# Optimization experiments

Hardware: AMD Instinct MI355X
Metric: run time of the kernel (lower is better)

The kernel has to match this reference:

```python
import jax, jax.numpy as jnp
import numpy as np
import math

B, TD, TP, D, H = 16, 256, 1024, 512, 8
DH = D // H
G_MIN = 0.05
LN_EPS = 1e-5
SCALE = 1.0 / math.sqrt(DH)


def _ln(x, g, b):
    m = jnp.mean(x, axis=-1, keepdims=True)
    v = jnp.var(x, axis=-1, keepdims=True)
    return (x - m) * jax.lax.rsqrt(v + LN_EPS) * g + b


def _evi(x, w1, b1, w2, b2, k):
    # EvidentialHead: Linear -> SiLU -> Linear(d->4), NIG params -> gate
    h = jax.nn.silu(x @ w1 + b1)
    p = h @ w2 + b2  # (B,T,4)
    gamma, nu, alpha, beta = jnp.split(p, 4, axis=-1)
    nu = jax.nn.softplus(nu) + 1e-6
    alpha = jax.nn.softplus(alpha) + 1.0
    beta = jax.nn.softplus(beta) + 1e-6
    sigma2 = beta / (nu * (alpha - 1.0))  # (B,T,1)
    g = jnp.clip(jnp.exp(-k * sigma2[..., 0]), G_MIN, 1.0)  # (B,T)
    return g


def _xattn(Q, KV, log_bias, wq, bq, wk, bk, wv, bv, wo, bo, lng, lnb):
    # Q: (B,M,D), KV: (B,N,D), log_bias: (B,N) added to logits pre-softmax
    Bq, M, _ = Q.shape
    N = KV.shape[1]
    q = (Q @ wq + bq).reshape(Bq, M, H, DH)
    k_ = (KV @ wk + bk).reshape(Bq, N, H, DH)
    v = (KV @ wv + bv).reshape(Bq, N, H, DH)
    scores = jnp.einsum('bmhd,bnhd->bhmn', q, k_) * SCALE
    scores = scores + log_bias[:, None, None, :]
    attn = jax.nn.softmax(scores, axis=-1)
    out = jnp.einsum('bhmn,bnhd->bmhd', attn, v).reshape(Bq, M, D)
    out = out @ wo + bo
    return _ln(Q + out, lng, lnb)


def _ffn(x, w1, b1, w2, b2, lng, lnb):
    # Linear(d,4d) -> SiLU -> Linear(4d,d) -> LayerNorm (no residual)
    h = jax.nn.silu(x @ w1 + b1)
    return _ln(h @ w2 + b2, lng, lnb)


def setup_inputs() -> dict:
    key = jax.random.key(0)
    ks = iter(jax.random.split(key, 64))

    def w(shape, s=0.02):
        return s * jax.random.normal(next(ks), shape, jnp.float32)

    def attn_params(pfx):
        p = {}
        for nm in ('wq', 'wk', 'wv', 'wo'):
            p[pfx + '_' + nm] = w((D, D))
        for nm in ('bq', 'bk', 'bv', 'bo'):
            p[pfx + '_' + nm] = jnp.zeros((D,), jnp.float32)
        p[pfx + '_lng'] = jnp.ones((D,), jnp.float32)
        p[pfx + '_lnb'] = jnp.zeros((D,), jnp.float32)
        return p

    def ffn_params(pfx):
        return {pfx + '_w1': w((D, 4 * D)), pfx + '_b1': jnp.zeros((4 * D,), jnp.float32),
                pfx + '_w2': w((4 * D, D)), pfx + '_b2': jnp.zeros((D,), jnp.float32),
                pfx + '_lng': jnp.ones((D,), jnp.float32), pfx + '_lnb': jnp.zeros((D,), jnp.float32)}

    inp = {
        'Hd': jax.random.normal(next(ks), (B, TD, D), jnp.float32),
        'Hp': jax.random.normal(next(ks), (B, TP, D), jnp.float32),
        'k': 1,
        'evid_w1': w((D, D)), 'evid_b1': jnp.zeros((D,), jnp.float32),
        'evid_w2': w((D, 4)), 'evid_b2': jnp.zeros((4,), jnp.float32),
        'evip_w1': w((D, D)), 'evip_b1': jnp.zeros((D,), jnp.float32),
        'evip_w2': w((D, 4)), 'evip_b2': jnp.zeros((4,), jnp.float32),
    }
    inp.update(attn_params('p2d'))
    inp.update(attn_params('d2p'))
    inp.update(ffn_params('ffnd'))
    inp.update(ffn_params('ffnp'))
    return inp


def reference(Hd, Hp, k,
              evid_w1, evid_b1, evid_w2, evid_b2,
              evip_w1, evip_b1, evip_w2, evip_b2,
              p2d_wq, p2d_wk, p2d_wv, p2d_wo, p2d_bq, p2d_bk, p2d_bv, p2d_bo, p2d_lng, p2d_lnb,
              d2p_wq, d2p_wk, d2p_wv, d2p_wo, d2p_bq, d2p_bk, d2p_bv, d2p_bo, d2p_lng, d2p_lnb,
              ffnd_w1, ffnd_b1, ffnd_w2, ffnd_b2, ffnd_lng, ffnd_lnb,
              ffnp_w1, ffnp_b1, ffnp_w2, ffnp_b2, ffnp_lng, ffnp_lnb):
    gd = _evi(Hd, evid_w1, evid_b1, evid_w2, evid_b2, k)  # (B,TD)
    gp = _evi(Hp, evip_w1, evip_b1, evip_w2, evip_b2, k)  # (B,TP)
    Hp2 = _xattn(Hp, Hd, jnp.log(gd + 1e-12),
                 p2d_wq, p2d_bq, p2d_wk, p2d_bk, p2d_wv, p2d_bv, p2d_wo, p2d_bo, p2d_lng, p2d_lnb)
    Hd2 = _xattn(Hd, Hp, jnp.log(gp + 1e-12),
                 d2p_wq, d2p_bq, d2p_wk, d2p_bk, d2p_wv, d2p_bv, d2p_wo, d2p_bo, d2p_lng, d2p_lnb)
    Hd_out = _ffn(Hd2, ffnd_w1, ffnd_b1, ffnd_w2, ffnd_b2, ffnd_lng, ffnd_lnb)
    Hp_out = _ffn(Hp2, ffnp_w1, ffnp_b1, ffnp_w2, ffnp_b2, ffnp_lng, ffnp_lnb)
    return (Hd_out, Hp_out, gd, gp)
```

## Files before the change

kernel.cpp:

```cpp
#include <hip/hip_runtime.h>
#include <stdint.h>
#include <math.h>

typedef unsigned short u16;
typedef __attribute__((ext_vector_type(8))) short bf16x8;
typedef __attribute__((ext_vector_type(8))) short short8;
typedef __attribute__((ext_vector_type(4))) float f32x4;
typedef __attribute__((ext_vector_type(4))) unsigned short u16x4;

#define NB 16
#define TDr 256
#define TPr 1024
#define DM 512
#define NH 8
#define DHEAD 64

__device__ __forceinline__ float us2f(u16 u) {
  union { float f; unsigned int i; } x; x.i = ((unsigned int)u) << 16; return x.f;
}
__device__ __forceinline__ u16 f2us(float f) {
  union { float fl; unsigned int i; } x; x.fl = f;
  unsigned int u = x.i;
  return (u16)((u + 0x7fffu + ((u >> 16) & 1u)) >> 16);
}

__global__ __launch_bounds__(64) void detect_kernel(const u16* __restrict__ raw,
                                                    int* __restrict__ flag)
{
  const int lane = threadIdx.x;
  float mx = 0.f;
  for (int i = lane; i < 256; i += 64) {
    float v = us2f(raw[i]);
    v = fabsf(v);
    if (isfinite(v)) mx = fmaxf(mx, v); else mx = 1e30f;
  }
#pragma unroll
  for (int o = 32; o; o >>= 1) mx = fmaxf(mx, __shfl_xor(mx, o));
  if (lane == 0) flag[0] = (mx > 1e10f) ? 1 : 0;
}

struct CvtDesc { const void* src; unsigned long dst_off; int n; };
struct CvtTable { CvtDesc d[42]; };

__global__ __launch_bounds__(256) void cvt_kernel(CvtTable t, u16* __restrict__ base,
                                                  const int* __restrict__ flag)
{
  const CvtDesc d = t.d[blockIdx.y];
  u16* dst = base + d.dst_off;
  const int isf32 = flag[0];
  const int stride = gridDim.x * 256;
  const int tid0 = blockIdx.x * 256 + threadIdx.x;
  if (d.n >= 8) {
    const int n8 = d.n >> 3;
    if (isf32) {
      const float* s = (const float*)d.src;
      for (int i = tid0; i < n8; i += stride) {
        f32x4 a = *(const f32x4*)&s[i * 8];
        f32x4 b = *(const f32x4*)&s[i * 8 + 4];
        short8 o;
        o[0]=(short)f2us(a[0]); o[1]=(short)f2us(a[1]); o[2]=(short)f2us(a[2]); o[3]=(short)f2us(a[3]);
        o[4]=(short)f2us(b[0]); o[5]=(short)f2us(b[1]); o[6]=(short)f2us(b[2]); o[7]=(short)f2us(b[3]);
        *(short8*)&dst[i * 8] = o;
      }
    } else {
      const short8* s = (const short8*)d.src;
      for (int i = tid0; i < n8; i += stride) *(short8*)&dst[i * 8] = s[i];
    }
  } else {
    if (isf32) {
      const float* s = (const float*)d.src;
      for (int i = tid0; i < d.n; i += stride) dst[i] = f2us(s[i]);
    } else {
      const u16* s = (const u16*)d.src;
      for (int i = tid0; i < d.n; i += stride) dst[i] = s[i];
    }
  }
}

template<int BM, int BN>
__device__ __forceinline__ void gemm_core(
    const u16* __restrict__ Ab, const u16* __restrict__ Bb,
    int K, int tid, f32x4 (&acc)[BM/32][BN/32])
{
  constexpr int BK = 32;
  constexpr int FM = BM / 32;
  constexpr int FN = BN / 32;
  constexpr int LPT = (BM * BK / 8 + BN * BK / 8) / 256;
  __shared__ __align__(16) u16 As[2][BM * BK];
  __shared__ __align__(16) u16 Bs[2][BN * BK];

  const int lane = tid & 63;
  const int wm = (tid >> 6) >> 1;
  const int wn = (tid >> 6) & 1;

#pragma unroll
  for (int i = 0; i < FM; ++i)
#pragma unroll
    for (int j = 0; j < FN; ++j)
      acc[i][j] = (f32x4){0.f, 0.f, 0.f, 0.f};

  auto stage = [&](int buf, int k0) {
#pragma unroll
    for (int c = tid; c < BM * BK / 8; c += 256) {
      const int r  = c >> 2;
      const int kk = (c & 3) << 3;
      __builtin_amdgcn_global_load_lds(
          (const __attribute__((address_space(1))) uint32_t*)(Ab + (long)r * K + k0 + kk),
          (__attribute__((address_space(3))) uint32_t*)(&As[buf][c * 8]), 16, 0, 0);
    }
#pragma unroll
    for (int c = tid; c < BN * BK / 8; c += 256) {
      const int r  = c >> 2;
      const int kk = (c & 3) << 3;
      __builtin_amdgcn_global_load_lds(
          (const __attribute__((address_space(1))) uint32_t*)(Bb + (long)r * K + k0 + kk),
          (__attribute__((address_space(3))) uint32_t*)(&Bs[buf][c * 8]), 16, 0, 0);
    }
  };

  const int nt = K / BK;
  stage(0, 0);
  if (nt > 1) stage(1, BK);

  for (int t = 0; t < nt; ++t) {
    if (t + 1 < nt) {
      if constexpr (LPT == 4) asm volatile("s_waitcnt vmcnt(4)" ::: "memory");
      else                    asm volatile("s_waitcnt vmcnt(3)" ::: "memory");
    } else {
      asm volatile("s_waitcnt vmcnt(0)" ::: "memory");
    }
    asm volatile("s_barrier" ::: "memory");
    __builtin_amdgcn_sched_barrier(0);

    const int cur = t & 1;
    bf16x8 af[FM], bfv[FN];
#pragma unroll
    for (int i = 0; i < FM; ++i)
      af[i] = *(const bf16x8*)&As[cur][(wm * (BM/2) + i*16 + (lane & 15)) * BK + ((lane >> 4) << 3)];
#pragma unroll
    for (int j = 0; j < FN; ++j)
      bfv[j] = *(const bf16x8*)&Bs[cur][(wn * (BN/2) + j*16 + (lane & 15)) * BK + ((lane >> 4) << 3)];
#pragma unroll
    for (int i = 0; i < FM; ++i)
#pragma unroll
      for (int j = 0; j < FN; ++j)
        acc[i][j] = __builtin_amdgcn_mfma_f32_16x16x32_bf16(af[i], bfv[j], acc[i][j], 0, 0, 0);

    __builtin_amdgcn_sched_barrier(0);
    asm volatile("s_barrier" ::: "memory");
    __builtin_amdgcn_sched_barrier(0);
    if (t + 2 < nt) stage(cur, (t + 2) * BK);
  }
}

struct ProjSet {
  const u16 *A, *W, *bE, *bQ, *bK, *bV;
  u16 *H, *Q, *Kc, *VT;
  int ntokLog, mtiles;
};

__global__ __launch_bounds__(256) void proj_pair(ProjSet s0, ProjSet s1)
{
  const ProjSet S = blockIdx.z ? s1 : s0;
  if ((int)blockIdx.x >= S.mtiles) return;
  const int tid = threadIdx.x;
  const int lane = tid & 63;
  const int wm = (tid >> 6) >> 1, wn = (tid >> 6) & 1;
  const int r16 = lane & 15, rr4 = (lane >> 4) << 2;
  const long row0 = (long)blockIdx.x * 128;
  const long col0 = (long)blockIdx.y * 128;

  f32x4 acc[4][4];
  gemm_core<128,128>(S.A + row0 * 512, S.W + col0 * 512, 512, tid, acc);

  const int range = (int)(col0 >> 9);
  const u16* bp = range == 0 ? S.bE : range == 1 ? S.bQ : range == 2 ? S.bK : S.bV;
  u16* dst = range == 0 ? S.H : range == 1 ? S.Q : S.Kc;
  const int ntok = 1 << S.ntokLog;

#pragma unroll
  for (int i = 0; i < 4; ++i) {
    const long gr0 = row0 + wm*64 + i*16 + rr4;
#pragma unroll
    for (int j = 0; j < 4; ++j) {
      const int cr = (int)(col0 & 511) + wn*64 + j*16 + r16;
      const float badd = us2f(bp[cr]);
      if (range == 3) {
        const long b = gr0 >> S.ntokLog;
        const long t0 = gr0 & (ntok - 1);
        u16x4 pk;
#pragma unroll
        for (int r = 0; r < 4; ++r) pk[r] = f2us(acc[i][j][r] + badd);
        *(u16x4*)&S.VT[((long)b * 512 + cr) * ntok + t0] = pk;
      } else if (range == 0) {
#pragma unroll
        for (int r = 0; r < 4; ++r) {
          float v = acc[i][j][r] + badd;
          v = v / (1.f + __expf(-v));
          dst[(gr0 + r) * 512 + cr] = f2us(v);
        }
      } else {
#pragma unroll
        for (int r = 0; r < 4; ++r)
          dst[(gr0 + r) * 512 + cr] = f2us(acc[i][j][r] + badd);
      }
    }
  }
}

struct Gm { const u16* A; const u16* Bt; const u16* bias; u16* C; int mtiles; };

template<int SILU>
__global__ __launch_bounds__(256) void gemm_pair(Gm g0, Gm g1, int ldc, int K)
{
  const Gm G = blockIdx.z ? g1 : g0;
  if ((int)blockIdx.x >= G.mtiles) return;
  const int tid = threadIdx.x;
  const int lane = tid & 63;
  const int wm = (tid >> 6) >> 1, wn = (tid >> 6) & 1;
  const int r16 = lane & 15, rr4 = (lane >> 4) << 2;
  const long row0 = (long)blockIdx.x * 128;
  const long col0 = (long)blockIdx.y * 128;

  f32x4 acc[4][4];
  gemm_core<128,128>(G.A + row0 * (long)K, G.Bt + col0 * (long)K, K, tid, acc);

#pragma unroll
  for (int i = 0; i < 4; ++i) {
    const long gr0 = row0 + wm*64 + i*16 + rr4;
#pragma unroll
    for (int j = 0; j < 4; ++j) {
      const long gc = col0 + wn*64 + j*16 + r16;
      const float badd = us2f(G.bias[gc]);
#pragma unroll
      for (int r = 0; r < 4; ++r) {
        float v = acc[i][j][r] + badd;
        if (SILU) v = v / (1.f + __expf(-v));
        G.C[(gr0 + r) * (long)ldc + gc] = f2us(v);
      }
    }
  }
}

template<int NKV, int RPW>
__global__ __launch_bounds__(256) void attn_fused(
    const u16* __restrict__ Qp, const u16* __restrict__ Kp,
    const u16* __restrict__ Vt, const float* __restrict__ lb,
    u16* __restrict__ Aout, int M)
{
  constexpr int NC = NKV >> 7;
  constexpr int FI = RPW / 16;
  constexpr int NS = 4 * FI;
  constexpr int QT = 4 * RPW;
  constexpr int PLD = 136;
  __shared__ __align__(16) u16 Ps[4][RPW][PLD];

  const int tid  = threadIdx.x;
  const int lane = tid & 63;
  const int w    = tid >> 6;
  const int bh = blockIdx.y;
  const int b = bh >> 3, h = bh & 7;
  const long q0 = (long)blockIdx.x * QT;

  const u16* Qb = Qp + ((long)b * M + q0) * DM + h * DHEAD;
  const u16* Kb = Kp + (long)b * NKV * DM + h * DHEAD;
  const u16* Vb = Vt + ((long)b * DM + h * DHEAD) * NKV;
  const float* lbb = lb + (long)b * NKV;

  const int r16 = lane & 15;
  const int k8  = (lane >> 4) << 3;
  const int rr4 = (lane >> 4) << 2;
  const float SCALE = 0.125f;

  bf16x8 qa[FI][2];
#pragma unroll
  for (int i = 0; i < FI; ++i)
#pragma unroll
    for (int kc = 0; kc < 2; ++kc)
      qa[i][kc] = *(const bf16x8*)&Qb[(long)(w*RPW + i*16 + r16) * DM + kc*32 + k8];

  f32x4 acc_o[FI][4];
#pragma unroll
  for (int i = 0; i < FI; ++i)
#pragma unroll
    for (int jo = 0; jo < 4; ++jo)
      acc_o[i][jo] = (f32x4){0.f, 0.f, 0.f, 0.f};
  float mrow[NS], lrow[NS];
#pragma unroll
  for (int s = 0; s < NS; ++s) { mrow[s] = -1e30f; lrow[s] = 0.f; }

#pragma unroll
  for (int c = 0; c < NC; ++c) {
    const int t0 = c * 128;
    f32x4 acc_s[FI][8];
#pragma unroll
    for (int i = 0; i < FI; ++i)
#pragma unroll
      for (int j = 0; j < 8; ++j)
        acc_s[i][j] = (f32x4){0.f, 0.f, 0.f, 0.f};
#pragma unroll
    for (int j = 0; j < 8; ++j) {
      const long trow = t0 + j*16 + r16;
      bf16x8 kb0 = *(const bf16x8*)&Kb[trow * DM + k8];
      bf16x8 kb1 = *(const bf16x8*)&Kb[trow * DM + 32 + k8];
#pragma unroll
      for (int i = 0; i < FI; ++i) {
        acc_s[i][j] = __builtin_amdgcn_mfma_f32_16x16x32_bf16(qa[i][0], kb0, acc_s[i][j], 0, 0, 0);
        acc_s[i][j] = __builtin_amdgcn_mfma_f32_16x16x32_bf16(qa[i][1], kb1, acc_s[i][j], 0, 0, 0);
      }
    }

    float lbv[8];
#pragma unroll
    for (int j = 0; j < 8; ++j) lbv[j] = lbb[t0 + j*16 + r16];
    float pm[NS];
#pragma unroll
    for (int s = 0; s < NS; ++s) pm[s] = -1e30f;
#pragma unroll
    for (int i = 0; i < FI; ++i)
#pragma unroll
      for (int j = 0; j < 8; ++j)
#pragma unroll
        for (int r = 0; r < 4; ++r) {
          float v = acc_s[i][j][r] * SCALE + lbv[j];
          acc_s[i][j][r] = v;
          pm[i*4 + r] = fmaxf(pm[i*4 + r], v);
        }
#pragma unroll
    for (int s = 0; s < NS; ++s) {
#pragma unroll
      for (int o = 1; o < 16; o <<= 1) pm[s] = fmaxf(pm[s], __shfl_xor(pm[s], o));
    }
    float sc[NS];
#pragma unroll
    for (int s = 0; s < NS; ++s) {
      const float mn = fmaxf(mrow[s], pm[s]);
      sc[s] = __expf(mrow[s] - mn);
      mrow[s] = mn;
      lrow[s] *= sc[s];
    }
#pragma unroll
    for (int i = 0; i < FI; ++i)
#pragma unroll
      for (int jo = 0; jo < 4; ++jo)
#pragma unroll
        for (int r = 0; r < 4; ++r)
          acc_o[i][jo][r] *= sc[i*4 + r];

    float ls[NS];
#pragma unroll
    for (int s = 0; s < NS; ++s) ls[s] = 0.f;
#pragma unroll
    for (int i = 0; i < FI; ++i)
#pragma unroll
      for (int j = 0; j < 8; ++j)
#pragma unroll
        for (int r = 0; r < 4; ++r) {
          const float p = __expf(acc_s[i][j][r] - mrow[i*4 + r]);
          ls[i*4 + r] += p;
          Ps[w][i*16 + rr4 + r][j*16 + r16] = f2us(p);
        }
#pragma unroll
    for (int s = 0; s < NS; ++s) {
#pragma unroll
      for (int o = 1; o < 16; o <<= 1) ls[s] += __shfl_xor(ls[s], o);
      lrow[s] += ls[s];
    }

    asm volatile("s_waitcnt lgkmcnt(0)" ::: "memory");
    __builtin_amdgcn_sched_barrier(0);

#pragma unroll
    for (int kc = 0; kc < 4; ++kc) {
      bf16x8 pa[FI];
#pragma unroll
      for (int i = 0; i < FI; ++i)
        pa[i] = *(const bf16x8*)&Ps[w][i*16 + r16][kc*32 + k8];
#pragma unroll
      for (int jo = 0; jo < 4; ++jo) {
        bf16x8 vb = *(const bf16x8*)&Vb[(long)(jo*16 + r16) * NKV + t0 + kc*32 + k8];
#pragma unroll
        for (int i = 0; i < FI; ++i)
          acc_o[i][jo] = __builtin_amdgcn_mfma_f32_16x16x32_bf16(pa[i], vb, acc_o[i][jo], 0, 0, 0);
      }
    }
    __builtin_amdgcn_sched_barrier(0);
  }

  float linv[NS];
#pragma unroll
  for (int s = 0; s < NS; ++s) linv[s] = 1.f / lrow[s];
  u16* Ob = Aout + ((long)b * M + q0) * DM + h * DHEAD;
#pragma unroll
  for (int i = 0; i < FI; ++i)
#pragma unroll
    for (int jo = 0; jo < 4; ++jo)
#pragma unroll
      for (int r = 0; r < 4; ++r) {
        const long row = w*RPW + i*16 + rr4 + r;
        Ob[row * DM + jo*16 + r16] = f2us(acc_o[i][jo][r] * linv[i*4 + r]);
      }
}

struct TTab { const u16* in; u16* out; int R, C; };
struct TTable { TTab d[14]; };

__global__ __launch_bounds__(256) void transpose_all(TTable tt)
{
  const TTab d = tt.d[blockIdx.z];
  __shared__ u16 t[32][33];
  const int tx = threadIdx.x & 31, ty = threadIdx.x >> 5;
  for (int r0 = blockIdx.y * 32; r0 < d.R; r0 += gridDim.y * 32) {
    for (int c0 = blockIdx.x * 32; c0 < d.C; c0 += gridDim.x * 32) {
#pragma unroll
      for (int i = 0; i < 4; ++i)
        t[ty + 8*i][tx] = d.in[(long)(r0 + ty + 8*i) * d.C + c0 + tx];
      __syncthreads();
#pragma unroll
      for (int i = 0; i < 4; ++i)
        d.out[(long)(c0 + ty + 8*i) * d.R + r0 + tx] = t[tx][ty + 8*i];
      __syncthreads();
    }
  }
}

struct LnR { const u16* X; const u16* P; const u16* g; const u16* b; u16* out; int rows; };

__global__ __launch_bounds__(256) void ln_res_pair(LnR a0, LnR a1)
{
  const LnR A = blockIdx.z ? a1 : a0;
  const int row = blockIdx.x * 4 + (threadIdx.x >> 6);
  if (row >= A.rows) return;
  const int lane = threadIdx.x & 63;
  const u16* pr = A.P + (long)row * DM;
  const u16* xr = A.X + (long)row * DM;
  float v[8], s = 0.f, s2 = 0.f;
#pragma unroll
  for (int i = 0; i < 8; ++i) {
    const int jx = i * 64 + lane;
    float t = us2f(pr[jx]) + us2f(xr[jx]);
    v[i] = t; s += t; s2 += t * t;
  }
#pragma unroll
  for (int o = 32; o; o >>= 1) { s += __shfl_xor(s, o); s2 += __shfl_xor(s2, o); }
  const float mean = s * (1.f / DM);
  const float var  = s2 * (1.f / DM) - mean * mean;
  const float rstd = rsqrtf(fmaxf(var, 0.f) + 1e-5f);
#pragma unroll
  for (int i = 0; i < 8; ++i) {
    const int jx = i * 64 + lane;
    A.out[(long)row * DM + jx] = f2us((v[i] - mean) * rstd * us2f(A.g[jx]) + us2f(A.b[jx]));
  }
}

struct LnF { const u16* P; const u16* g; const u16* b; long oofs; int rows; };

__global__ __launch_bounds__(256) void ln_final_pair(LnF a0, LnF a1,
                                                     void* __restrict__ outb,
                                                     const int* __restrict__ flag)
{
  const LnF A = blockIdx.z ? a1 : a0;
  const int row = blockIdx.x * 4 + (threadIdx.x >> 6);
  if (row >= A.rows) return;
  const int lane = threadIdx.x & 63;
  const u16* pr = A.P + (long)row * DM;
  float v[8], s = 0.f, s2 = 0.f;
#pragma unroll
  for (int i = 0; i < 8; ++i) {
    const int jx = i * 64 + lane;
    float t = us2f(pr[jx]);
    v[i] = t; s += t; s2 += t * t;
  }
#pragma unroll
  for (int o = 32; o; o >>= 1) { s += __shfl_xor(s, o); s2 += __shfl_xor(s2, o); }
  const float mean = s * (1.f / DM);
  const float var  = s2 * (1.f / DM) - mean * mean;
  const float rstd = rsqrtf(fmaxf(var, 0.f) + 1e-5f);
  const int isf32 = flag[0];
#pragma unroll
  for (int i = 0; i < 8; ++i) {
    const int jx = i * 64 + lane;
    const float ov = (v[i] - mean) * rstd * us2f(A.g[jx]) + us2f(A.b[jx]);
    if (isf32) ((float*)outb)[A.oofs + (long)row * DM + jx] = ov;
    else       ((u16*)outb)[A.oofs + (long)row * DM + jx] = f2us(ov);
  }
}

struct Gt { const u16* H; const u16* W2; const u16* b2; long oofs; float* lb; int rows; };

__global__ __launch_bounds__(256) void gate_pair(Gt a0, Gt a1,
                                                 const int* __restrict__ kptr,
                                                 void* __restrict__ outb,
                                                 const int* __restrict__ flag)
{
  const Gt A = blockIdx.z ? a1 : a0;
  const int row = blockIdx.x * 4 + (threadIdx.x >> 6);
  if (row >= A.rows) return;
  const int lane = threadIdx.x & 63;
  const u16* hr = A.H + (long)row * DM;
  float p1 = 0.f, p2 = 0.f, p3 = 0.f;
#pragma unroll
  for (int i = 0; i < 8; ++i) {
    const int idx = i * 64 + lane;
    const float hv = us2f(hr[idx]);
    const u16x4 w = *(const u16x4*)&A.W2[idx * 4];
    p1 += hv * us2f(w[1]);
    p2 += hv * us2f(w[2]); p3 += hv * us2f(w[3]);
  }
#pragma unroll
  for (int o = 32; o; o >>= 1) {
    p1 += __shfl_xor(p1, o);
    p2 += __shfl_xor(p2, o); p3 += __shfl_xor(p3, o);
  }
  if (lane == 0) {
    const float nu = p1 + us2f(A.b2[1]);
    const float al = p2 + us2f(A.b2[2]);
    const float be = p3 + us2f(A.b2[3]);
    auto sp = [](float x) { return x > 20.f ? x : log1pf(expf(x)); };
    const float spn = sp(nu) + 1e-6f;
    const float spa = sp(al);
    const float spb = sp(be) + 1e-6f;
    const float sig = spb / (spn * spa);
    const float kk = (float)kptr[0];
    float gg = expf(-kk * sig);
    gg = fminf(fmaxf(gg, 0.05f), 1.f);
    if (flag[0]) ((float*)outb)[A.oofs + row] = gg;
    else         ((u16*)outb)[A.oofs + row] = f2us(gg);
    A.lb[row] = logf(gg + 1e-12f);
  }
}

extern "C" void kernel_launch(void* const* d_in, const int* in_sizes, int n_in,
                              void* d_out, int out_size, void* d_ws, size_t ws_size,
                              hipStream_t stream)
{
  const int* kptr = (const int*)d_in[2];

  uint8_t* base = (uint8_t*)d_ws;
  size_t off = 0;
  auto take = [&](size_t bytes) -> void* {
    void* p = base + off;
    off += (bytes + 255) & ~(size_t)255;
    return p;
  };
  int* FLAG = (int*)take(256);

  const int sizes[42] = {
    2097152, 8388608,
    262144, 512, 2048, 4,
    262144, 512, 2048, 4,
    262144,262144,262144,262144, 512,512,512,512, 512,512,
    262144,262144,262144,262144, 512,512,512,512, 512,512,
    1048576, 2048, 1048576, 512, 512, 512,
    1048576, 2048, 1048576, 512, 512, 512
  };
  u16* canon[42];
  u16* cbase = (u16*)take(17319944ul * 2 + 256);
  {
    unsigned long coff = 0;
    for (int i = 0; i < 42; ++i) {
      canon[i] = cbase + coff;
      coff += (unsigned long)((sizes[i] + 7) & ~7);
    }
  }
  const u16 *HdC = canon[0], *HpC = canon[1];
  const u16 *evid_w1 = canon[2], *evid_b1 = canon[3], *evid_w2 = canon[4], *evid_b2 = canon[5];
  const u16 *evip_w1 = canon[6], *evip_b1 = canon[7], *evip_w2 = canon[8], *evip_b2 = canon[9];
  const u16 *p2d_wq = canon[10], *p2d_wk = canon[11], *p2d_wv = canon[12], *p2d_wo = canon[13];
  const u16 *p2d_bq = canon[14], *p2d_bk = canon[15], *p2d_bv = canon[16], *p2d_bo = canon[17];
  const u16 *p2d_lng = canon[18], *p2d_lnb = canon[19];
  const u16 *d2p_wq = canon[20], *d2p_wk = canon[21], *d2p_wv = canon[22], *d2p_wo = canon[23];
  const u16 *d2p_bq = canon[24], *d2p_bk = canon[25], *d2p_bv = canon[26], *d2p_bo = canon[27];
  const u16 *d2p_lng = canon[28], *d2p_lnb = canon[29];
  const u16 *ffnd_w1 = canon[30], *ffnd_b1 = canon[31], *ffnd_w2 = canon[32], *ffnd_b2 = canon[33];
  const u16 *ffnd_lng = canon[34], *ffnd_lnb = canon[35];
  const u16 *ffnp_w1 = canon[36], *ffnp_b1 = canon[37], *ffnp_w2 = canon[38], *ffnp_b2 = canon[39];
  const u16 *ffnp_lng = canon[40], *ffnp_lnb = canon[41];

  u16* HpW = (u16*)take((size_t)2048*512*2);
  u16* HdW = (u16*)take((size_t)2048*512*2);
  u16* woT_p = (u16*)take((size_t)512*512*2);
  u16* woT_d = (u16*)take((size_t)512*512*2);
  u16* ffnp_w1T = (u16*)take((size_t)2048*512*2);
  u16* ffnp_w2T = (u16*)take((size_t)512*2048*2);
  u16* ffnd_w1T = (u16*)take((size_t)2048*512*2);
  u16* ffnd_w2T = (u16*)take((size_t)512*2048*2);

  u16* HBUF_p = (u16*)take((size_t)16384*512*2);
  u16* HBUF_d = (u16*)take((size_t)4096*512*2);
  u16* QBUF_p = (u16*)take((size_t)16384*512*2);
  u16* QBUF_d = (u16*)take((size_t)4096*512*2);
  u16* KBUF_p = (u16*)take((size_t)16384*512*2);
  u16* KBUF_d = (u16*)take((size_t)4096*512*2);
  u16* VT_p   = (u16*)take((size_t)16384*512*2);
  u16* VT_d   = (u16*)take((size_t)4096*512*2);
  u16* ABUF_p = (u16*)take((size_t)16384*512*2);
  u16* ABUF_d = (u16*)take((size_t)4096*512*2);
  u16* HP2  = (u16*)take((size_t)16384*512*2);
  u16* HD2  = (u16*)take((size_t)4096*512*2);
  float* LBD  = (float*)take((size_t)NB*TDr*4);
  float* LBP  = (float*)take((size_t)NB*TPr*4);
  if (off > ws_size) return;

  u16* PBUF_p = HBUF_p;
  u16* PBUF_d = HBUF_d;
  u16* SBUF_p = QBUF_p;
  u16* SBUF_d = SBUF_p + (size_t)16384*2048;

  const long O_HD = 0;
  const long O_HP = 2097152;
  const long O_GD = 10485760;
  const long O_GP = 10489856;

  detect_kernel<<<dim3(1), 64, 0, stream>>>((const u16*)d_in[0], FLAG);
  CvtTable tbl;
  {
    int ii = 0;
    for (int i = 0; i < 43; ++i) {
      if (i == 2) continue;
      tbl.d[ii].src = d_in[i];
      tbl.d[ii].dst_off = (unsigned long)(canon[ii] - cbase);
      tbl.d[ii].n = sizes[ii];
      ++ii;
    }
  }
  cvt_kernel<<<dim3(64, 42), 256, 0, stream>>>(tbl, cbase, FLAG);

  TTable tt;
  {
    const TTab tts[14] = {
      {evip_w1, HpW + 0*512*512, 512, 512},
      {p2d_wq,  HpW + 1*512*512, 512, 512},
      {d2p_wk,  HpW + 2*512*512, 512, 512},
      {d2p_wv,  HpW + 3*512*512, 512, 512},
      {evid_w1, HdW + 0*512*512, 512, 512},
      {d2p_wq,  HdW + 1*512*512, 512, 512},
      {p2d_wk,  HdW + 2*512*512, 512, 512},
      {p2d_wv,  HdW + 3*512*512, 512, 512},
      {p2d_wo, woT_p, 512, 512}, {d2p_wo, woT_d, 512, 512},
      {ffnp_w1, ffnp_w1T, 512, 2048}, {ffnp_w2, ffnp_w2T, 2048, 512},
      {ffnd_w1, ffnd_w1T, 512, 2048}, {ffnd_w2, ffnd_w2T, 2048, 512},
    };
    for (int i = 0; i < 14; ++i) tt.d[i] = tts[i];
  }
  transpose_all<<<dim3(16, 16, 14), 256, 0, stream>>>(tt);

  ProjSet sp{HpC, HpW, evip_b1, p2d_bq, d2p_bk, d2p_bv,
             HBUF_p, QBUF_p, KBUF_p, VT_p, 10, 128};
  ProjSet sd{HdC, HdW, evid_b1, d2p_bq, p2d_bk, p2d_bv,
             HBUF_d, QBUF_d, KBUF_d, VT_d, 8, 32};
  proj_pair<<<dim3(128, 16, 2), 256, 0, stream>>>(sp, sd);

  Gt gp{HBUF_p, evip_w2, evip_b2, O_GP, LBP, 16384};
  Gt gd{HBUF_d, evid_w2, evid_b2, O_GD, LBD, 4096};
  gate_pair<<<dim3(4096, 1, 2), 256, 0, stream>>>(gp, gd, kptr, d_out, FLAG);

  attn_fused<TDr,32><<<dim3(TPr/128, NB*NH), 256, 0, stream>>>(
      QBUF_p, KBUF_d, VT_d, LBD, ABUF_p, TPr);
  attn_fused<TPr,16><<<dim3(TDr/64, NB*NH), 256, 0, stream>>>(
      QBUF_d, KBUF_p, VT_p, LBP, ABUF_d, TDr);

  Gm wp{ABUF_p, woT_p, p2d_bo, PBUF_p, 128};
  Gm wd{ABUF_d, woT_d, d2p_bo, PBUF_d, 32};
  gemm_pair<0><<<dim3(128, 4, 2), 256, 0, stream>>>(wp, wd, 512, 512);

  LnR lp{HpC, PBUF_p, p2d_lng, p2d_lnb, HP2, 16384};
  LnR ld{HdC, PBUF_d, d2p_lng, d2p_lnb, HD2, 4096};
  ln_res_pair<<<dim3(4096, 1, 2), 256, 0, stream>>>(lp, ld);

  Gm f1p{HP2, ffnp_w1T, ffnp_b1, SBUF_p, 128};
  Gm f1d{HD2, ffnd_w1T, ffnd_b1, SBUF_d, 32};
  gemm_pair<1><<<dim3(128, 16, 2), 256, 0, stream>>>(f1p, f1d, 2048, 512);

  Gm f2p{SBUF_p, ffnp_w2T, ffnp_b2, PBUF_p, 128};
  Gm f2d{SBUF_d, ffnd_w2T, ffnd_b2, PBUF_d, 32};
  gemm_pair<0><<<dim3(128, 4, 2), 256, 0, stream>>>(f2p, f2d, 512, 2048);

  LnF fp{PBUF_p, ffnp_lng, ffnp_lnb, O_HP, 16384};
  LnF fd{PBUF_d, ffnd_lng, ffnd_lnb, O_HD, 4096};
  ln_final_pair<<<dim3(4096, 1, 2), 256, 0, stream>>>(fp, fd, d_out, FLAG);
}
```

Baseline: 438.5 us.

## Double GEMM K-tile to 64 and XOR-swizzle LDS layout

The GEMM core now stages K tiles of 64 instead of 32, which halves the number of barrier and wait steps per K loop. The LDS tile is stored with an XOR swizzle of 16-byte chunks by row, and fragment reads index through the same swizzle to avoid bank conflicts. The wait count is hard-coded to vmcnt(8), which assumes BM equals BN (4 loads per tile per thread). LDS use doubles, which may lower occupancy.

```diff
diff --git a/kernel.cpp b/kernel.cpp
--- a/kernel.cpp
+++ b/kernel.cpp
@@ -82,16 +82,18 @@
     const u16* __restrict__ Ab, const u16* __restrict__ Bb,
     int K, int tid, f32x4 (&acc)[BM/32][BN/32])
 {
-  constexpr int BK = 32;
+  constexpr int BK = 64;
   constexpr int FM = BM / 32;
   constexpr int FN = BN / 32;
-  constexpr int LPT = (BM * BK / 8 + BN * BK / 8) / 256;
+  constexpr int CPT = BM * BK / 8 / 256;
   __shared__ __align__(16) u16 As[2][BM * BK];
   __shared__ __align__(16) u16 Bs[2][BN * BK];
 
   const int lane = tid & 63;
   const int wm = (tid >> 6) >> 1;
   const int wn = (tid >> 6) & 1;
+  const int r16 = lane & 15;
+  const int l4  = lane >> 4;
 
 #pragma unroll
   for (int i = 0; i < FM; ++i)
@@ -101,19 +103,21 @@
 
   auto stage = [&](int buf, int k0) {
 #pragma unroll
-    for (int c = tid; c < BM * BK / 8; c += 256) {
-      const int r  = c >> 2;
-      const int kk = (c & 3) << 3;
+    for (int it = 0; it < CPT; ++it) {
+      const int c = tid + it * 256;
+      const int r = c >> 3;
+      const int src = (c & 7) ^ (r & 7);
       __builtin_amdgcn_global_load_lds(
-          (const __attribute__((address_space(1))) uint32_t*)(Ab + (long)r * K + k0 + kk),
+          (const __attribute__((address_space(1))) uint32_t*)(Ab + (long)r * K + k0 + src * 8),
           (__attribute__((address_space(3))) uint32_t*)(&As[buf][c * 8]), 16, 0, 0);
     }
 #pragma unroll
-    for (int c = tid; c < BN * BK / 8; c += 256) {
-      const int r  = c >> 2;
-      const int kk = (c & 3) << 3;
+    for (int it = 0; it < CPT; ++it) {
+      const int c = tid + it * 256;
+      const int r = c >> 3;
+      const int src = (c & 7) ^ (r & 7);
       __builtin_amdgcn_global_load_lds(
-          (const __attribute__((address_space(1))) uint32_t*)(Bb + (long)r * K + k0 + kk),
+          (const __attribute__((address_space(1))) uint32_t*)(Bb + (long)r * K + k0 + src * 8),
           (__attribute__((address_space(3))) uint32_t*)(&Bs[buf][c * 8]), 16, 0, 0);
     }
   };
@@ -124,8 +128,7 @@
 
   for (int t = 0; t < nt; ++t) {
     if (t + 1 < nt) {
-      if constexpr (LPT == 4) asm volatile("s_waitcnt vmcnt(4)" ::: "memory");
-      else                    asm volatile("s_waitcnt vmcnt(3)" ::: "memory");
+      asm volatile("s_waitcnt vmcnt(8)" ::: "memory");
     } else {
       asm volatile("s_waitcnt vmcnt(0)" ::: "memory");
     }
@@ -133,18 +136,26 @@
     __builtin_amdgcn_sched_barrier(0);
 
     const int cur = t & 1;
-    bf16x8 af[FM], bfv[FN];
-#pragma unroll
-    for (int i = 0; i < FM; ++i)
-      af[i] = *(const bf16x8*)&As[cur][(wm * (BM/2) + i*16 + (lane & 15)) * BK + ((lane >> 4) << 3)];
-#pragma unroll
-    for (int j = 0; j < FN; ++j)
-      bfv[j] = *(const bf16x8*)&Bs[cur][(wn * (BN/2) + j*16 + (lane & 15)) * BK + ((lane >> 4) << 3)];
-#pragma unroll
-    for (int i = 0; i < FM; ++i)
-#pragma unroll
-      for (int j = 0; j < FN; ++j)
-        acc[i][j] = __builtin_amdgcn_mfma_f32_16x16x32_bf16(af[i], bfv[j], acc[i][j], 0, 0, 0);
+#pragma unroll
+    for (int kh = 0; kh < 2; ++kh) {
+      const int kc = kh * 4 + l4;
+      bf16x8 af[FM], bfv[FN];
+#pragma unroll
+      for (int i = 0; i < FM; ++i) {
+        const int row = wm * (BM/2) + i*16 + r16;
+        af[i] = *(const bf16x8*)&As[cur][(row << 6) + ((kc ^ (row & 7)) << 3)];
+      }
+#pragma unroll
+      for (int j = 0; j < FN; ++j) {
+        const int row = wn * (BN/2) + j*16 + r16;
+        bfv[j] = *(const bf16x8*)&Bs[cur][(row << 6) + ((kc ^ (row & 7)) << 3)];
+      }
+#pragma unroll
+      for (int i = 0; i < FM; ++i)
+#pragma unroll
+        for (int j = 0; j < FN; ++j)
+          acc[i][j] = __builtin_amdgcn_mfma_f32_16x16x32_bf16(af[i], bfv[j], acc[i][j], 0, 0, 0);
+    }
 
     __builtin_amdgcn_sched_barrier(0);
     asm volatile("s_barrier" ::: "memory");
```

After: 451.8 us. 1.03x slower.
